# Kernel optimization log

Hardware: AMD Instinct MI355X
Metric: run time of the kernel (lower is better)

## Reference

```python
import jax, jax.numpy as jnp
import numpy as np

N = 20000
E = 320000
F_IN = 256
NHID = 64
H1 = 8
H2 = 1
NUM_CLASSES = 40
NEG_SLOPE = 0.2


def setup_inputs() -> dict:
    key = jax.random.key(0)
    ks = jax.random.split(key, 11)
    glorot = lambda k, shape: jax.random.normal(k, shape, jnp.float32) * jnp.sqrt(2.0 / (shape[0] + shape[-1]))
    x = jax.random.normal(ks[0], (N, F_IN), jnp.float32)
    edge_index = jax.random.randint(ks[1], (2, E), 0, N, jnp.int64)
    W1 = glorot(ks[2], (F_IN, H1 * NHID))
    att_src1 = glorot(ks[3], (H1, NHID))
    att_dst1 = glorot(ks[4], (H1, NHID))
    b1 = jnp.zeros((H1 * NHID,), jnp.float32)
    W2 = glorot(ks[5], (H1 * NHID, H2 * NUM_CLASSES))
    att_src2 = glorot(ks[6], (H2, NUM_CLASSES))
    att_dst2 = glorot(ks[7], (H2, NUM_CLASSES))
    b2 = jnp.zeros((NUM_CLASSES,), jnp.float32)
    return {"x": x, "edge_index": edge_index, "W1": W1, "att_src1": att_src1,
            "att_dst1": att_dst1, "b1": b1, "W2": W2, "att_src2": att_src2,
            "att_dst2": att_dst2, "b2": b2}


def gat_conv(x, src, dst, W, a_src, a_dst, bias, concat):
    # x: [N, F_in], src/dst: [E'] (self-loops already appended)
    H, C = a_src.shape
    h = (x @ W).reshape(N, H, C)                       # [N,H,C]
    alpha_src = jnp.sum(h * a_src, axis=-1)            # [N,H]
    alpha_dst = jnp.sum(h * a_dst, axis=-1)            # [N,H]
    e = jax.nn.leaky_relu(alpha_src[src] + alpha_dst[dst], NEG_SLOPE)  # [E',H]
    # segment softmax over incoming edges of each dst node
    emax = jax.lax.stop_gradient(jax.ops.segment_max(e, dst, num_segments=N))
    ee = jnp.exp(e - emax[dst])
    denom = jax.ops.segment_sum(ee, dst, num_segments=N)
    alpha = ee / (denom[dst] + 1e-16)                  # [E',H]
    out = jax.ops.segment_sum(alpha[:, :, None] * h[src], dst, num_segments=N)  # [N,H,C]
    out = out.reshape(N, H * C) if concat else out.mean(axis=1)
    return out + bias


def reference(x, edge_index, W1, att_src1, att_dst1, b1, W2, att_src2, att_dst2, b2):
    # PyG GATConv adds self-loops by default
    loops = jnp.arange(N, dtype=edge_index.dtype)
    src = jnp.concatenate([edge_index[0], loops])
    dst = jnp.concatenate([edge_index[1], loops])
    h = gat_conv(x, src, dst, W1, att_src1, att_dst1, b1, concat=True)   # [N, H1*NHID]
    h = jax.nn.elu(h)
    out = gat_conv(h, src, dst, W2, att_src2, att_dst2, b2, concat=False)  # [N, NUM_CLASSES]
    return jax.nn.log_softmax(out, axis=1)
```

## Files before the change

kernel.cpp:

```cpp
#include <hip/hip_runtime.h>
#include <hip/hip_bf16.h>
#include <math.h>

#define N_NODES 20000
#define MPAD 20096
#define N_EDGES 320000
#define EP (N_EDGES + N_NODES)
#define F_IN 256
#define NHID 64
#define H1 8
#define D1 512
#define NCLS 40
#define NEG_SLOPE 0.2f
#define MAXD 128

typedef __attribute__((ext_vector_type(8))) short bf16x8;
typedef __attribute__((ext_vector_type(4))) float f32x4;

__device__ __forceinline__ float wave_max(float v) {
#pragma unroll
  for (int o = 32; o > 0; o >>= 1) v = fmaxf(v, __shfl_xor(v, o));
  return v;
}
__device__ __forceinline__ float wave_sum(float v) {
#pragma unroll
  for (int o = 32; o > 0; o >>= 1) v += __shfl_xor(v, o);
  return v;
}
__device__ __forceinline__ unsigned short f2bf(float f) {
  union { float f; unsigned int i; } c; c.f = f;
  unsigned int x = c.i;
  return (unsigned short)((x + 0x7fffu + ((x >> 16) & 1u)) >> 16);
}
__device__ __forceinline__ float asf(unsigned int u) {
  union { unsigned int i; float f; } c; c.i = u; return c.f;
}
__device__ __forceinline__ float lrelu(float x) { return x > 0.f ? x : NEG_SLOPE * x; }

__device__ __forceinline__ void gload16(const void* g, void* l) {
  __builtin_amdgcn_global_load_lds((const __attribute__((address_space(1))) void*)g,
                                   (__attribute__((address_space(3))) void*)l, 16, 0, 0);
}

#define PB_CONV 2512
#define PB_TW1  (PB_CONV + 32)
#define PB_TW2  (PB_TW1 + 96)
#define PB_ZERO (PB_TW2 + 157)
#define PB_PAD  (PB_ZERO + 24)
__global__ __launch_bounds__(256) void prep_kernel(const float* __restrict__ x,
                                                   const float* __restrict__ W1,
                                                   const float* __restrict__ W2,
                                                   unsigned short* __restrict__ xb,
                                                   unsigned short* __restrict__ wb1t,
                                                   unsigned short* __restrict__ wb2t,
                                                   int* __restrict__ deg,
                                                   int* __restrict__ cursor,
                                                   unsigned short* __restrict__ out1b) {
  __shared__ float tsh[64][65];
  int bid = blockIdx.x;
  int t = threadIdx.x;
  if (bid < PB_CONV) {
    size_t base = ((size_t)bid * 256 + t) * 8;
    int row = (int)(base >> 8);
    ushort4 o0, o1;
    if (row < N_NODES) {
      float4 v0 = *(const float4*)&x[base];
      float4 v1 = *(const float4*)&x[base + 4];
      o0 = make_ushort4(f2bf(v0.x), f2bf(v0.y), f2bf(v0.z), f2bf(v0.w));
      o1 = make_ushort4(f2bf(v1.x), f2bf(v1.y), f2bf(v1.z), f2bf(v1.w));
    } else {
      o0 = make_ushort4(0, 0, 0, 0); o1 = o0;
    }
    *(ushort4*)&xb[base] = o0;
    *(ushort4*)&xb[base + 4] = o1;
  } else if (bid < PB_TW1) {
    int b2 = bid - PB_CONV;
    int bk = b2 & 3, bn = b2 >> 2;
    int tr = t >> 4, tc4 = (t & 15) * 4;
#pragma unroll
    for (int i = 0; i < 4; ++i) {
      int k = i * 16 + tr;
      float4 v = *(const float4*)&W1[(size_t)(bk * 64 + k) * D1 + bn * 64 + tc4];
      tsh[k][tc4] = v.x; tsh[k][tc4 + 1] = v.y; tsh[k][tc4 + 2] = v.z; tsh[k][tc4 + 3] = v.w;
    }
    __syncthreads();
#pragma unroll
    for (int i = 0; i < 4; ++i) {
      int n = i * 16 + tr;
      ushort4 o = make_ushort4(f2bf(tsh[tc4][n]), f2bf(tsh[tc4 + 1][n]),
                               f2bf(tsh[tc4 + 2][n]), f2bf(tsh[tc4 + 3][n]));
      *(ushort4*)&wb1t[(size_t)(bn * 64 + n) * F_IN + bk * 64 + tc4] = o;
    }
  } else if (bid < PB_TW2) {
    int idx = (bid - PB_TW1) * 256 + t;
    int c = idx >> 9, k = idx & 511;
    wb2t[idx] = f2bf((c < NCLS) ? W2[(size_t)k * NCLS + c] : 0.f);
  } else if (bid < PB_ZERO) {
    int idx = (bid - PB_TW2) * 256 + t;
    if (idx < N_NODES) deg[idx] = 0;
    else if (idx < 2 * N_NODES) cursor[idx - N_NODES] = 0;
  } else {
    int idx = (bid - PB_ZERO) * 256 + t;
    uint4 z = make_uint4(0, 0, 0, 0);
    *(uint4*)((char*)out1b + (size_t)N_NODES * D1 * 2 + (size_t)idx * 16) = z;
  }
}

__global__ void count_deg(const int* __restrict__ ei, int* __restrict__ deg) {
  int e = blockIdx.x * blockDim.x + threadIdx.x;
  if (e >= EP) return;
  int dst = (e < N_EDGES) ? ei[N_EDGES + e] : (e - N_EDGES);
  atomicAdd(&deg[dst], 1);
}

#define SCAN_T 1024
#define SCAN_CHUNK 20
__global__ __launch_bounds__(1024) void scan_kernel(const int* __restrict__ deg,
                                                    int* __restrict__ offsets) {
  __shared__ int wsum[16];
  int t = threadIdx.x;
  int w = t >> 6, lane = t & 63;
  int lo = t * SCAN_CHUNK;
  int hi = min(lo + SCAN_CHUNK, N_NODES);
  int s = 0;
  for (int i = lo; i < hi; ++i) s += deg[i];
  int incl = s;
#pragma unroll
  for (int o = 1; o < 64; o <<= 1) {
    int v = __shfl_up(incl, o);
    if (lane >= o) incl += v;
  }
  if (lane == 63) wsum[w] = incl;
  __syncthreads();
  if (t == 0) {
    int run = 0;
#pragma unroll
    for (int i = 0; i < 16; ++i) { int v = wsum[i]; wsum[i] = run; run += v; }
  }
  __syncthreads();
  int off = wsum[w] + incl - s;
  for (int i = lo; i < hi; ++i) { offsets[i] = off; off += deg[i]; }
  if (hi == N_NODES && lo < N_NODES) offsets[N_NODES] = off;
}

__global__ void scatter_edges(const int* __restrict__ ei, const int* __restrict__ offsets,
                              int* __restrict__ cursor, int* __restrict__ edge_src) {
  int e = blockIdx.x * blockDim.x + threadIdx.x;
  if (e >= EP) return;
  int src, dst;
  if (e < N_EDGES) { src = ei[e]; dst = ei[N_EDGES + e]; }
  else             { src = dst = e - N_EDGES; }
  int pos = offsets[dst] + atomicAdd(&cursor[dst], 1);
  edge_src[pos] = src;
}

__global__ __launch_bounds__(256) void gemm1_mfma(const unsigned short* __restrict__ xb,
                                                  const unsigned short* __restrict__ wb1t,
                                                  const float* __restrict__ a_src,
                                                  const float* __restrict__ a_dst,
                                                  unsigned short* __restrict__ h1b,
                                                  float* __restrict__ asrc,
                                                  float* __restrict__ adst) {
  __shared__ unsigned short As[128 * 64];
  __shared__ unsigned short Bs[128 * 64];
  int tid = threadIdx.x;
  int w = tid >> 6, lane = tid & 63;
  int bn = blockIdx.x & 3, bm = blockIdx.x >> 2;
  int row0 = bm * 128, col0 = bn * 128;
  int wr = w >> 1, wc = w & 1;
  int cl = lane & 15, hi = lane >> 4;
  f32x4 acc[4][4] = {};
  for (int k0 = 0; k0 < F_IN; k0 += 64) {
#pragma unroll
    for (int c = 0; c < 4; ++c) {
      int slot = c * 256 + tid;
      int r = slot >> 3;
      int q = (slot & 7) ^ (r & 7);
      gload16(xb + (size_t)(row0 + r) * F_IN + k0 + q * 8, (char*)As + (c * 256 + w * 64) * 16);
      gload16(wb1t + (size_t)(col0 + r) * F_IN + k0 + q * 8, (char*)Bs + (c * 256 + w * 64) * 16);
    }
    __syncthreads();
#pragma unroll
    for (int kk = 0; kk < 2; ++kk) {
      bf16x8 a[4], b[4];
#pragma unroll
      for (int m = 0; m < 4; ++m) {
        int r = wr * 64 + m * 16 + cl;
        a[m] = *(const bf16x8*)&As[r * 64 + ((((kk * 4 + hi)) ^ (r & 7)) << 3)];
      }
#pragma unroll
      for (int n = 0; n < 4; ++n) {
        int r = wc * 64 + n * 16 + cl;
        b[n] = *(const bf16x8*)&Bs[r * 64 + ((((kk * 4 + hi)) ^ (r & 7)) << 3)];
      }
#pragma unroll
      for (int m = 0; m < 4; ++m)
#pragma unroll
        for (int n = 0; n < 4; ++n)
          acc[m][n] = __builtin_amdgcn_mfma_f32_16x16x32_bf16(a[m], b[n], acc[m][n], 0, 0, 0);
    }
    __syncthreads();
  }
  int head = bn * 2 + wc;
  float asv[4], adv[4];
#pragma unroll
  for (int n = 0; n < 4; ++n) {
    asv[n] = a_src[head * 64 + n * 16 + cl];
    adv[n] = a_dst[head * 64 + n * 16 + cl];
  }
#pragma unroll
  for (int m = 0; m < 4; ++m) {
#pragma unroll
    for (int r = 0; r < 4; ++r) {
      int grow = row0 + wr * 64 + m * 16 + hi * 4 + r;
      float ps = acc[m][0][r] * asv[0] + acc[m][1][r] * asv[1] +
                 acc[m][2][r] * asv[2] + acc[m][3][r] * asv[3];
      float pd = acc[m][0][r] * adv[0] + acc[m][1][r] * adv[1] +
                 acc[m][2][r] * adv[2] + acc[m][3][r] * adv[3];
#pragma unroll
      for (int o = 8; o > 0; o >>= 1) { ps += __shfl_xor(ps, o); pd += __shfl_xor(pd, o); }
      if (grow < N_NODES) {
#pragma unroll
        for (int n = 0; n < 4; ++n)
          h1b[(size_t)grow * D1 + col0 + wc * 64 + n * 16 + cl] = f2bf(acc[m][n][r]);
        if (cl == 0) { asrc[grow * H1 + head] = ps; adst[grow * H1 + head] = pd; }
      }
    }
  }
}

__global__ __launch_bounds__(256) void alpha1_kernel(const int* __restrict__ offsets,
                                                     const int* __restrict__ edge_src,
                                                     const float* __restrict__ asrc,
                                                     const float* __restrict__ adst,
                                                     float* __restrict__ alphaE,
                                                     float* __restrict__ inv1) {
  int w = threadIdx.x >> 6, lane = threadIdx.x & 63;
  int n = blockIdx.x * 4 + w;
  int base = offsets[n];
  int deg = offsets[n + 1] - base;
  int h = lane & 7, et = lane >> 3;
  float adv = adst[n * H1 + h];
  float evr[8];
  float m = -INFINITY;
#pragma unroll
  for (int k = 0; k < 8; ++k) {
    int e = et + k * 8;
    float ev = -INFINITY;
    if (e < deg) ev = lrelu(asrc[edge_src[base + e] * H1 + h] + adv);
    evr[k] = ev;
    m = fmaxf(m, ev);
  }
  for (int e = et + 64; e < deg; e += 8)
    m = fmaxf(m, lrelu(asrc[edge_src[base + e] * H1 + h] + adv));
  m = fmaxf(m, __shfl_xor(m, 8));
  m = fmaxf(m, __shfl_xor(m, 16));
  m = fmaxf(m, __shfl_xor(m, 32));
  float ss = 0.f;
#pragma unroll
  for (int k = 0; k < 8; ++k) {
    int e = et + k * 8;
    if (e < deg) {
      float a = __expf(evr[k] - m);
      alphaE[(size_t)h * EP + base + e] = a;
      ss += a;
    }
  }
  for (int e = et + 64; e < deg; e += 8) {
    float a = __expf(lrelu(asrc[edge_src[base + e] * H1 + h] + adv) - m);
    alphaE[(size_t)h * EP + base + e] = a;
    ss += a;
  }
  ss += __shfl_xor(ss, 8);
  ss += __shfl_xor(ss, 16);
  ss += __shfl_xor(ss, 32);
  if (et == 0) inv1[n * H1 + h] = 1.f / (ss + 1e-16f);
}

__global__ __launch_bounds__(256) void agg1_gather(const int* __restrict__ offsets,
                                                   const int* __restrict__ edge_src,
                                                   const float* __restrict__ alphaE,
                                                   const float* __restrict__ inv1,
                                                   const unsigned short* __restrict__ h1b,
                                                   const float* __restrict__ b1,
                                                   unsigned short* __restrict__ out1b) {
  int w = threadIdx.x >> 6, lane = threadIdx.x & 63;
  int bid = blockIdx.x;
  int head = bid & 7;
  int ng = bid >> 3;
  int sub = lane >> 3, cl = lane & 7;
  int n = ng * 32 + w * 8 + sub;
  int base = offsets[n];
  int deg = offsets[n + 1] - base;
  const float* aE = alphaE + (size_t)head * EP + base;
  const int* es = edge_src + base;
  const char* hb = (const char*)h1b + head * 128 + cl * 16;
  float acc[8] = {};
  int e = 0;
  for (; e + 3 < deg; e += 4) {
    float a0 = aE[e], a1 = aE[e + 1], a2 = aE[e + 2], a3 = aE[e + 3];
    int s0 = es[e], s1 = es[e + 1], s2 = es[e + 2], s3 = es[e + 3];
    uint4 u0 = *(const uint4*)(hb + ((size_t)s0 << 10));
    uint4 u1 = *(const uint4*)(hb + ((size_t)s1 << 10));
    uint4 u2 = *(const uint4*)(hb + ((size_t)s2 << 10));
    uint4 u3 = *(const uint4*)(hb + ((size_t)s3 << 10));
#pragma unroll
    for (int j = 0; j < 4; ++j) {
      unsigned int x0 = ((const unsigned int*)&u0)[j];
      unsigned int x1 = ((const unsigned int*)&u1)[j];
      unsigned int x2 = ((const unsigned int*)&u2)[j];
      unsigned int x3 = ((const unsigned int*)&u3)[j];
      acc[2 * j]     += a0 * asf(x0 << 16) + a1 * asf(x1 << 16)
                      + a2 * asf(x2 << 16) + a3 * asf(x3 << 16);
      acc[2 * j + 1] += a0 * asf(x0 & 0xffff0000u) + a1 * asf(x1 & 0xffff0000u)
                      + a2 * asf(x2 & 0xffff0000u) + a3 * asf(x3 & 0xffff0000u);
    }
  }
  for (; e < deg; ++e) {
    float a = aE[e];
    int s = es[e];
    uint4 uv = *(const uint4*)(hb + ((size_t)s << 10));
#pragma unroll
    for (int j = 0; j < 4; ++j) {
      unsigned int u = ((const unsigned int*)&uv)[j];
      acc[2 * j]     += a * asf(u << 16);
      acc[2 * j + 1] += a * asf(u & 0xffff0000u);
    }
  }
  float inv = inv1[n * H1 + head];
  int c0 = head * NHID + cl * 8;
  float4 b0 = *(const float4*)&b1[c0];
  float4 b4 = *(const float4*)&b1[c0 + 4];
  float v[8];
  v[0] = acc[0] * inv + b0.x; v[1] = acc[1] * inv + b0.y;
  v[2] = acc[2] * inv + b0.z; v[3] = acc[3] * inv + b0.w;
  v[4] = acc[4] * inv + b4.x; v[5] = acc[5] * inv + b4.y;
  v[6] = acc[6] * inv + b4.z; v[7] = acc[7] * inv + b4.w;
#pragma unroll
  for (int j = 0; j < 8; ++j) v[j] = v[j] > 0.f ? v[j] : (__expf(v[j]) - 1.f);
  ushort4 o0 = make_ushort4(f2bf(v[0]), f2bf(v[1]), f2bf(v[2]), f2bf(v[3]));
  ushort4 o1 = make_ushort4(f2bf(v[4]), f2bf(v[5]), f2bf(v[6]), f2bf(v[7]));
  *(ushort4*)&out1b[(size_t)n * D1 + c0] = o0;
  *(ushort4*)&out1b[(size_t)n * D1 + c0 + 4] = o1;
}

__global__ __launch_bounds__(256) void gemm2_mfma(const unsigned short* __restrict__ ab,
                                                  const unsigned short* __restrict__ wb2t,
                                                  const float* __restrict__ a_src2,
                                                  const float* __restrict__ a_dst2,
                                                  float* __restrict__ h2,
                                                  float* __restrict__ asrc,
                                                  float* __restrict__ adst) {
  __shared__ unsigned short As[64 * 64];
  __shared__ unsigned short Bs[48 * 64];
  int tid = threadIdx.x;
  int w = tid >> 6, lane = tid & 63;
  int row0 = blockIdx.x * 64;
  int cl = lane & 15, hi = lane >> 4;
  f32x4 acc[3] = {};
  for (int k0 = 0; k0 < D1; k0 += 64) {
#pragma unroll
    for (int c = 0; c < 2; ++c) {
      int slot = c * 256 + tid;
      int r = slot >> 3;
      int q = (slot & 7) ^ (r & 7);
      gload16(ab + (size_t)(row0 + r) * D1 + k0 + q * 8, (char*)As + (c * 256 + w * 64) * 16);
    }
    {
      int r = tid >> 3;
      int q = (tid & 7) ^ (r & 7);
      gload16(wb2t + (size_t)r * D1 + k0 + q * 8, (char*)Bs + (w * 64) * 16);
      if (tid < 128) {
        int slot2 = 256 + tid;
        int r2 = slot2 >> 3;
        int q2 = (slot2 & 7) ^ (r2 & 7);
        gload16(wb2t + (size_t)r2 * D1 + k0 + q2 * 8, (char*)Bs + ((256 + w * 64)) * 16);
      }
    }
    __syncthreads();
#pragma unroll
    for (int kk = 0; kk < 2; ++kk) {
      int ra = w * 16 + cl;
      bf16x8 a = *(const bf16x8*)&As[ra * 64 + (((kk * 4 + hi) ^ (ra & 7)) << 3)];
#pragma unroll
      for (int n = 0; n < 3; ++n) {
        int rb = n * 16 + cl;
        bf16x8 b = *(const bf16x8*)&Bs[rb * 64 + (((kk * 4 + hi) ^ (rb & 7)) << 3)];
        acc[n] = __builtin_amdgcn_mfma_f32_16x16x32_bf16(a, b, acc[n], 0, 0, 0);
      }
    }
    __syncthreads();
  }
  float asv[3], adv[3];
#pragma unroll
  for (int n = 0; n < 3; ++n) {
    int c = n * 16 + cl;
    asv[n] = (c < NCLS) ? a_src2[c] : 0.f;
    adv[n] = (c < NCLS) ? a_dst2[c] : 0.f;
  }
#pragma unroll
  for (int r = 0; r < 4; ++r) {
    int grow = row0 + w * 16 + hi * 4 + r;
    float ps = acc[0][r] * asv[0] + acc[1][r] * asv[1] + acc[2][r] * asv[2];
    float pd = acc[0][r] * adv[0] + acc[1][r] * adv[1] + acc[2][r] * adv[2];
#pragma unroll
    for (int o = 8; o > 0; o >>= 1) { ps += __shfl_xor(ps, o); pd += __shfl_xor(pd, o); }
    if (grow < N_NODES) {
#pragma unroll
      for (int n = 0; n < 3; ++n) {
        int c = n * 16 + cl;
        if (c < NCLS) h2[(size_t)grow * NCLS + c] = acc[n][r];
      }
      if (cl == 0) { asrc[grow] = ps; adst[grow] = pd; }
    }
  }
}

__global__ __launch_bounds__(256) void agg2_kernel(const int* __restrict__ offsets,
                                                   const int* __restrict__ edge_src,
                                                   const float* __restrict__ asrc,
                                                   const float* __restrict__ adst,
                                                   const float* __restrict__ h2,
                                                   const float* __restrict__ b2,
                                                   float* __restrict__ out) {
  __shared__ float lalpha[4][MAXD + 8];
  __shared__ int   lsoff[4][MAXD + 8];
  int w = threadIdx.x >> 6;
  int lane = threadIdx.x & 63;
  int n = blockIdx.x * 4 + w;
  int base = offsets[n];
  int deg = offsets[n + 1] - base;
  int degc = min(deg, MAXD);
  int degp = ((degc + 5) / 6) * 6;

  float advv = adst[n];
  float m = -INFINITY;
  for (int e = lane; e < deg; e += 64) {
    int s = edge_src[base + e];
    float ev = lrelu(asrc[s] + advv);
    if (e < MAXD) { lsoff[w][e] = s * (NCLS * 4); lalpha[w][e] = ev; }
    m = fmaxf(m, ev);
  }
  m = wave_max(m);
  float ssum = 0.f;
  for (int e = lane; e < deg; e += 64) {
    float ev;
    if (e < MAXD) ev = lalpha[w][e];
    else { int s = edge_src[base + e]; ev = lrelu(asrc[s] + advv); }
    ssum += __expf(ev - m);
  }
  float inv = 1.f / (wave_sum(ssum) + 1e-16f);
  for (int e = lane; e < degc; e += 64) lalpha[w][e] = __expf(lalpha[w][e] - m) * inv;
  {
    int e = degc + lane;
    if (e < degp) { lalpha[w][e] = 0.f; lsoff[w][e] = 0; }
  }
  __builtin_amdgcn_wave_barrier();

  int esub = lane / 20;
  int cg = lane - esub * 20;
  bool act = esub < 3;
  float ax = 0.f, ay = 0.f;
  const char* hb = (const char*)h2 + cg * 8;
  for (int i = 0; i < degp; i += 6) {
    if (act) {
      int sA = i + esub, sB = i + 3 + esub;
      float aA = lalpha[w][sA], aB = lalpha[w][sB];
      int oA = lsoff[w][sA], oB = lsoff[w][sB];
      float2 hA = *(const float2*)(hb + oA);
      float2 hB = *(const float2*)(hb + oB);
      ax += aA * hA.x + aB * hB.x;
      ay += aA * hA.y + aB * hB.y;
    }
  }
  for (int e = MAXD + esub; e < deg; e += 3) {
    if (act) {
      int s = edge_src[base + e];
      float a = __expf(lrelu(asrc[s] + advv) - m) * inv;
      float2 hv = *(const float2*)(hb + (size_t)s * (NCLS * 4));
      ax += a * hv.x; ay += a * hv.y;
    }
  }
  float ax1 = __shfl(ax, lane + 20), ax2 = __shfl(ax, lane + 40);
  float ay1 = __shfl(ay, lane + 20), ay2 = __shfl(ay, lane + 40);
  float v0 = -INFINITY, v1 = -INFINITY;
  if (lane < 20) {
    v0 = ax + ax1 + ax2 + b2[2 * cg];
    v1 = ay + ay1 + ay2 + b2[2 * cg + 1];
  }
  float m2 = wave_max(fmaxf(v0, v1));
  float se = wave_sum(lane < 20 ? __expf(v0 - m2) + __expf(v1 - m2) : 0.f);
  if (lane < 20) {
    float ls = logf(se);
    *(float2*)&out[(size_t)n * NCLS + 2 * cg] = make_float2(v0 - m2 - ls, v1 - m2 - ls);
  }
}

extern "C" void kernel_launch(void* const* d_in, const int* in_sizes, int n_in,
                              void* d_out, int out_size, void* d_ws, size_t ws_size,
                              hipStream_t stream) {
  const float* x   = (const float*)d_in[0];
  const int*   ei  = (const int*)d_in[1];
  const float* W1  = (const float*)d_in[2];
  const float* as1 = (const float*)d_in[3];
  const float* ad1 = (const float*)d_in[4];
  const float* b1  = (const float*)d_in[5];
  const float* W2  = (const float*)d_in[6];
  const float* as2 = (const float*)d_in[7];
  const float* ad2 = (const float*)d_in[8];
  const float* b2  = (const float*)d_in[9];
  float* out = (float*)d_out;

  char* ws = (char*)d_ws;
  size_t off = 0;
  auto alloc = [&](size_t bytes) -> char* {
    char* p = ws + off;
    off += (bytes + 255) & ~(size_t)255;
    return p;
  };
  int* deg      = (int*)alloc((size_t)N_NODES * 4);
  int* cursor   = (int*)alloc((size_t)N_NODES * 4);
  int* offsets  = (int*)alloc((size_t)(N_NODES + 1) * 4);
  int* edge_src = (int*)alloc((size_t)EP * 4);
  unsigned short* xb    = (unsigned short*)alloc((size_t)MPAD * F_IN * 2);
  unsigned short* wb1t  = (unsigned short*)alloc((size_t)D1 * F_IN * 2);
  unsigned short* wb2t  = (unsigned short*)alloc((size_t)48 * D1 * 2);
  unsigned short* h1b   = (unsigned short*)alloc((size_t)N_NODES * D1 * 2);
  unsigned short* out1b = (unsigned short*)alloc((size_t)MPAD * D1 * 2);
  float* asrc1  = (float*)alloc((size_t)N_NODES * H1 * 4);
  float* adst1  = (float*)alloc((size_t)N_NODES * H1 * 4);
  float* alphaE = (float*)alloc((size_t)H1 * EP * 4);
  float* inv1   = (float*)alloc((size_t)N_NODES * H1 * 4);
  float* h2     = (float*)alloc((size_t)N_NODES * NCLS * 4);
  float* asrc2  = (float*)alloc((size_t)N_NODES * 4);
  float* adst2  = (float*)alloc((size_t)N_NODES * 4);

  prep_kernel<<<PB_PAD, 256, 0, stream>>>(x, W1, W2, xb, wb1t, wb2t, deg, cursor, out1b);
  count_deg<<<(EP + 255) / 256, 256, 0, stream>>>(ei, deg);
  scan_kernel<<<1, SCAN_T, 0, stream>>>(deg, offsets);
  scatter_edges<<<(EP + 255) / 256, 256, 0, stream>>>(ei, offsets, cursor, edge_src);

  gemm1_mfma<<<157 * 4, 256, 0, stream>>>(xb, wb1t, as1, ad1, h1b, asrc1, adst1);
  alpha1_kernel<<<N_NODES / 4, 256, 0, stream>>>(offsets, edge_src, asrc1, adst1, alphaE, inv1);
  agg1_gather<<<(N_NODES / 32) * 8, 256, 0, stream>>>(offsets, edge_src, alphaE, inv1, h1b, b1, out1b);

  gemm2_mfma<<<MPAD / 64, 256, 0, stream>>>(out1b, wb2t, as2, ad2, h2, asrc2, adst2);
  agg2_kernel<<<N_NODES / 4, 256, 0, stream>>>(offsets, edge_src, asrc2, adst2, h2, b2, out);
}
```

Before: 154.1 us.

## Sort nodes by degree for agg1 gather to balance wave work

Builds a degree histogram in the scan kernel and a new scatter_perm kernel that produces a node permutation bucketed by in-degree (capped at 63). agg1_gather processes nodes through this permutation, so the eight nodes sharing a wave have similar degrees and less lane divergence. The gather tail is also unrolled by two. This adds an extra small kernel launch and an indirection load, and scatter order within a bin is non-deterministic. Output locality is reduced because neighbouring lanes now write to scattered rows.

```diff
diff --git a/kernel.cpp b/kernel.cpp
--- a/kernel.cpp
+++ b/kernel.cpp
@@ -116,14 +116,23 @@
 #define SCAN_T 1024
 #define SCAN_CHUNK 20
 __global__ __launch_bounds__(1024) void scan_kernel(const int* __restrict__ deg,
-                                                    int* __restrict__ offsets) {
+                                                    int* __restrict__ offsets,
+                                                    int* __restrict__ binoff,
+                                                    int* __restrict__ bincur) {
   __shared__ int wsum[16];
+  __shared__ int hist[64];
   int t = threadIdx.x;
   int w = t >> 6, lane = t & 63;
+  if (t < 64) hist[t] = 0;
+  __syncthreads();
   int lo = t * SCAN_CHUNK;
   int hi = min(lo + SCAN_CHUNK, N_NODES);
   int s = 0;
-  for (int i = lo; i < hi; ++i) s += deg[i];
+  for (int i = lo; i < hi; ++i) {
+    int d = deg[i];
+    s += d;
+    atomicAdd(&hist[min(d, 63)], 1);
+  }
   int incl = s;
 #pragma unroll
   for (int o = 1; o < 64; o <<= 1) {
@@ -136,7 +145,12 @@
     int run = 0;
 #pragma unroll
     for (int i = 0; i < 16; ++i) { int v = wsum[i]; wsum[i] = run; run += v; }
-  }
+    int brun = 0;
+#pragma unroll
+    for (int i = 0; i < 64; ++i) { int v = hist[i]; binoff[i] = brun; brun += v; }
+    binoff[64] = brun;
+  }
+  if (t < 64) bincur[t] = 0;
   __syncthreads();
   int off = wsum[w] + incl - s;
   for (int i = lo; i < hi; ++i) { offsets[i] = off; off += deg[i]; }
@@ -152,6 +166,15 @@
   else             { src = dst = e - N_EDGES; }
   int pos = offsets[dst] + atomicAdd(&cursor[dst], 1);
   edge_src[pos] = src;
+}
+
+__global__ void scatter_perm(const int* __restrict__ offsets, const int* __restrict__ binoff,
+                             int* __restrict__ bincur, int* __restrict__ perm) {
+  int n = blockIdx.x * blockDim.x + threadIdx.x;
+  if (n >= N_NODES) return;
+  int d = min(offsets[n + 1] - offsets[n], 63);
+  int pos = binoff[d] + atomicAdd(&bincur[d], 1);
+  perm[pos] = n;
 }
 
 __global__ __launch_bounds__(256) void gemm1_mfma(const unsigned short* __restrict__ xb,
@@ -279,6 +302,7 @@
 
 __global__ __launch_bounds__(256) void agg1_gather(const int* __restrict__ offsets,
                                                    const int* __restrict__ edge_src,
+                                                   const int* __restrict__ perm,
                                                    const float* __restrict__ alphaE,
                                                    const float* __restrict__ inv1,
                                                    const unsigned short* __restrict__ h1b,
@@ -289,7 +313,7 @@
   int head = bid & 7;
   int ng = bid >> 3;
   int sub = lane >> 3, cl = lane & 7;
-  int n = ng * 32 + w * 8 + sub;
+  int n = perm[ng * 32 + w * 8 + sub];
   int base = offsets[n];
   int deg = offsets[n + 1] - base;
   const float* aE = alphaE + (size_t)head * EP + base;
@@ -316,7 +340,21 @@
                       + a2 * asf(x2 & 0xffff0000u) + a3 * asf(x3 & 0xffff0000u);
     }
   }
-  for (; e < deg; ++e) {
+  if (e + 1 < deg) {
+    float a0 = aE[e], a1 = aE[e + 1];
+    int s0 = es[e], s1 = es[e + 1];
+    uint4 u0 = *(const uint4*)(hb + ((size_t)s0 << 10));
+    uint4 u1 = *(const uint4*)(hb + ((size_t)s1 << 10));
+#pragma unroll
+    for (int j = 0; j < 4; ++j) {
+      unsigned int x0 = ((const unsigned int*)&u0)[j];
+      unsigned int x1 = ((const unsigned int*)&u1)[j];
+      acc[2 * j]     += a0 * asf(x0 << 16) + a1 * asf(x1 << 16);
+      acc[2 * j + 1] += a0 * asf(x0 & 0xffff0000u) + a1 * asf(x1 & 0xffff0000u);
+    }
+    e += 2;
+  }
+  if (e < deg) {
     float a = aE[e];
     int s = es[e];
     uint4 uv = *(const uint4*)(hb + ((size_t)s << 10));
@@ -522,6 +560,9 @@
   int* cursor   = (int*)alloc((size_t)N_NODES * 4);
   int* offsets  = (int*)alloc((size_t)(N_NODES + 1) * 4);
   int* edge_src = (int*)alloc((size_t)EP * 4);
+  int* binoff   = (int*)alloc(65 * 4);
+  int* bincur   = (int*)alloc(64 * 4);
+  int* perm     = (int*)alloc((size_t)N_NODES * 4);
   unsigned short* xb    = (unsigned short*)alloc((size_t)MPAD * F_IN * 2);
   unsigned short* wb1t  = (unsigned short*)alloc((size_t)D1 * F_IN * 2);
   unsigned short* wb2t  = (unsigned short*)alloc((size_t)48 * D1 * 2);
@@ -537,12 +578,13 @@
 
   prep_kernel<<<PB_PAD, 256, 0, stream>>>(x, W1, W2, xb, wb1t, wb2t, deg, cursor, out1b);
   count_deg<<<(EP + 255) / 256, 256, 0, stream>>>(ei, deg);
-  scan_kernel<<<1, SCAN_T, 0, stream>>>(deg, offsets);
+  scan_kernel<<<1, SCAN_T, 0, stream>>>(deg, offsets, binoff, bincur);
   scatter_edges<<<(EP + 255) / 256, 256, 0, stream>>>(ei, offsets, cursor, edge_src);
+  scatter_perm<<<(N_NODES + 255) / 256, 256, 0, stream>>>(offsets, binoff, bincur, perm);
 
   gemm1_mfma<<<157 * 4, 256, 0, stream>>>(xb, wb1t, as1, ad1, h1b, asrc1, adst1);
   alpha1_kernel<<<N_NODES / 4, 256, 0, stream>>>(offsets, edge_src, asrc1, adst1, alphaE, inv1);
-  agg1_gather<<<(N_NODES / 32) * 8, 256, 0, stream>>>(offsets, edge_src, alphaE, inv1, h1b, b1, out1b);
+  agg1_gather<<<(N_NODES / 32) * 8, 256, 0, stream>>>(offsets, edge_src, perm, alphaE, inv1, h1b, b1, out1b);
 
   gemm2_mfma<<<MPAD / 64, 256, 0, stream>>>(out1b, wb2t, as2, ad2, h2, asrc2, adst2);
   agg2_kernel<<<N_NODES / 4, 256, 0, stream>>>(offsets, edge_src, asrc2, adst2, h2, b2, out);
```

Result: slower. 217.2 us (+40.9%).

## Fuse degree count into prep kernel and edge scatter into gemm1 launch

Applied to the files above, without the earlier changes.

The degree-count pass moves into extra blocks of the prep kernel, and the CSR scatter moves into extra blocks of the gemm1 launch. The zeroing of deg and cursor becomes two hipMemsetAsync calls. This removes two kernel launches and lets the independent graph-building work overlap with the conversion and GEMM work. The agg1 gather loop is also unrolled to 8 edges, with 4/2/1 tails, to keep more gather loads in flight. The costs are two memset operations and heavier register use in the aggregation kernel.

```diff
diff --git a/kernel.cpp b/kernel.cpp
--- a/kernel.cpp
+++ b/kernel.cpp
@@ -45,16 +45,16 @@
 #define PB_CONV 2512
 #define PB_TW1  (PB_CONV + 32)
 #define PB_TW2  (PB_TW1 + 96)
-#define PB_ZERO (PB_TW2 + 157)
-#define PB_PAD  (PB_ZERO + 24)
+#define PB_PAD  (PB_TW2 + 24)
+#define PB_CNT  (PB_PAD + 1329)
 __global__ __launch_bounds__(256) void prep_kernel(const float* __restrict__ x,
                                                    const float* __restrict__ W1,
                                                    const float* __restrict__ W2,
+                                                   const int* __restrict__ ei,
                                                    unsigned short* __restrict__ xb,
                                                    unsigned short* __restrict__ wb1t,
                                                    unsigned short* __restrict__ wb2t,
                                                    int* __restrict__ deg,
-                                                   int* __restrict__ cursor,
                                                    unsigned short* __restrict__ out1b) {
   __shared__ float tsh[64][65];
   int bid = blockIdx.x;
@@ -95,22 +95,17 @@
     int idx = (bid - PB_TW1) * 256 + t;
     int c = idx >> 9, k = idx & 511;
     wb2t[idx] = f2bf((c < NCLS) ? W2[(size_t)k * NCLS + c] : 0.f);
-  } else if (bid < PB_ZERO) {
+  } else if (bid < PB_PAD) {
     int idx = (bid - PB_TW2) * 256 + t;
-    if (idx < N_NODES) deg[idx] = 0;
-    else if (idx < 2 * N_NODES) cursor[idx - N_NODES] = 0;
-  } else {
-    int idx = (bid - PB_ZERO) * 256 + t;
     uint4 z = make_uint4(0, 0, 0, 0);
     *(uint4*)((char*)out1b + (size_t)N_NODES * D1 * 2 + (size_t)idx * 16) = z;
-  }
-}
-
-__global__ void count_deg(const int* __restrict__ ei, int* __restrict__ deg) {
-  int e = blockIdx.x * blockDim.x + threadIdx.x;
-  if (e >= EP) return;
-  int dst = (e < N_EDGES) ? ei[N_EDGES + e] : (e - N_EDGES);
-  atomicAdd(&deg[dst], 1);
+  } else {
+    int e = (bid - PB_PAD) * 256 + t;
+    if (e < EP) {
+      int dst = (e < N_EDGES) ? ei[N_EDGES + e] : (e - N_EDGES);
+      atomicAdd(&deg[dst], 1);
+    }
+  }
 }
 
 #define SCAN_T 1024
@@ -143,27 +138,32 @@
   if (hi == N_NODES && lo < N_NODES) offsets[N_NODES] = off;
 }
 
-__global__ void scatter_edges(const int* __restrict__ ei, const int* __restrict__ offsets,
-                              int* __restrict__ cursor, int* __restrict__ edge_src) {
-  int e = blockIdx.x * blockDim.x + threadIdx.x;
-  if (e >= EP) return;
-  int src, dst;
-  if (e < N_EDGES) { src = ei[e]; dst = ei[N_EDGES + e]; }
-  else             { src = dst = e - N_EDGES; }
-  int pos = offsets[dst] + atomicAdd(&cursor[dst], 1);
-  edge_src[pos] = src;
-}
-
+#define G1_BLOCKS 628
 __global__ __launch_bounds__(256) void gemm1_mfma(const unsigned short* __restrict__ xb,
                                                   const unsigned short* __restrict__ wb1t,
                                                   const float* __restrict__ a_src,
                                                   const float* __restrict__ a_dst,
                                                   unsigned short* __restrict__ h1b,
                                                   float* __restrict__ asrc,
-                                                  float* __restrict__ adst) {
+                                                  float* __restrict__ adst,
+                                                  const int* __restrict__ ei,
+                                                  const int* __restrict__ offsets,
+                                                  int* __restrict__ cursor,
+                                                  int* __restrict__ edge_src) {
   __shared__ unsigned short As[128 * 64];
   __shared__ unsigned short Bs[128 * 64];
   int tid = threadIdx.x;
+  if (blockIdx.x >= G1_BLOCKS) {
+    int e = (blockIdx.x - G1_BLOCKS) * 256 + tid;
+    if (e < EP) {
+      int src, dst;
+      if (e < N_EDGES) { src = ei[e]; dst = ei[N_EDGES + e]; }
+      else             { src = dst = e - N_EDGES; }
+      int pos = offsets[dst] + atomicAdd(&cursor[dst], 1);
+      edge_src[pos] = src;
+    }
+    return;
+  }
   int w = tid >> 6, lane = tid & 63;
   int bn = blockIdx.x & 3, bm = blockIdx.x >> 2;
   int row0 = bm * 128, col0 = bn * 128;
@@ -297,26 +297,55 @@
   const char* hb = (const char*)h1b + head * 128 + cl * 16;
   float acc[8] = {};
   int e = 0;
+  for (; e + 7 < deg; e += 8) {
+    float av[8]; int sv[8];
+#pragma unroll
+    for (int q = 0; q < 8; ++q) { av[q] = aE[e + q]; sv[q] = es[e + q]; }
+    uint4 uv[8];
+#pragma unroll
+    for (int q = 0; q < 8; ++q) uv[q] = *(const uint4*)(hb + ((size_t)sv[q] << 10));
+#pragma unroll
+    for (int q = 0; q < 8; ++q) {
+#pragma unroll
+      for (int j = 0; j < 4; ++j) {
+        unsigned int u = ((const unsigned int*)&uv[q])[j];
+        acc[2 * j]     += av[q] * asf(u << 16);
+        acc[2 * j + 1] += av[q] * asf(u & 0xffff0000u);
+      }
+    }
+  }
   for (; e + 3 < deg; e += 4) {
-    float a0 = aE[e], a1 = aE[e + 1], a2 = aE[e + 2], a3 = aE[e + 3];
-    int s0 = es[e], s1 = es[e + 1], s2 = es[e + 2], s3 = es[e + 3];
+    float av[4]; int sv[4];
+#pragma unroll
+    for (int q = 0; q < 4; ++q) { av[q] = aE[e + q]; sv[q] = es[e + q]; }
+    uint4 uv[4];
+#pragma unroll
+    for (int q = 0; q < 4; ++q) uv[q] = *(const uint4*)(hb + ((size_t)sv[q] << 10));
+#pragma unroll
+    for (int q = 0; q < 4; ++q) {
+#pragma unroll
+      for (int j = 0; j < 4; ++j) {
+        unsigned int u = ((const unsigned int*)&uv[q])[j];
+        acc[2 * j]     += av[q] * asf(u << 16);
+        acc[2 * j + 1] += av[q] * asf(u & 0xffff0000u);
+      }
+    }
+  }
+  if (e + 1 < deg) {
+    float a0 = aE[e], a1 = aE[e + 1];
+    int s0 = es[e], s1 = es[e + 1];
     uint4 u0 = *(const uint4*)(hb + ((size_t)s0 << 10));
     uint4 u1 = *(const uint4*)(hb + ((size_t)s1 << 10));
-    uint4 u2 = *(const uint4*)(hb + ((size_t)s2 << 10));
-    uint4 u3 = *(const uint4*)(hb + ((size_t)s3 << 10));
 #pragma unroll
     for (int j = 0; j < 4; ++j) {
       unsigned int x0 = ((const unsigned int*)&u0)[j];
       unsigned int x1 = ((const unsigned int*)&u1)[j];
-      unsigned int x2 = ((const unsigned int*)&u2)[j];
-      unsigned int x3 = ((const unsigned int*)&u3)[j];
-      acc[2 * j]     += a0 * asf(x0 << 16) + a1 * asf(x1 << 16)
-                      + a2 * asf(x2 << 16) + a3 * asf(x3 << 16);
-      acc[2 * j + 1] += a0 * asf(x0 & 0xffff0000u) + a1 * asf(x1 & 0xffff0000u)
-                      + a2 * asf(x2 & 0xffff0000u) + a3 * asf(x3 & 0xffff0000u);
-    }
-  }
-  for (; e < deg; ++e) {
+      acc[2 * j]     += a0 * asf(x0 << 16) + a1 * asf(x1 << 16);
+      acc[2 * j + 1] += a0 * asf(x0 & 0xffff0000u) + a1 * asf(x1 & 0xffff0000u);
+    }
+    e += 2;
+  }
+  if (e < deg) {
     float a = aE[e];
     int s = es[e];
     uint4 uv = *(const uint4*)(hb + ((size_t)s << 10));
@@ -535,12 +564,13 @@
   float* asrc2  = (float*)alloc((size_t)N_NODES * 4);
   float* adst2  = (float*)alloc((size_t)N_NODES * 4);
 
-  prep_kernel<<<PB_PAD, 256, 0, stream>>>(x, W1, W2, xb, wb1t, wb2t, deg, cursor, out1b);
-  count_deg<<<(EP + 255) / 256, 256, 0, stream>>>(ei, deg);
+  hipMemsetAsync(deg, 0, (size_t)N_NODES * 4, stream);
+  hipMemsetAsync(cursor, 0, (size_t)N_NODES * 4, stream);
+
+  prep_kernel<<<PB_CNT, 256, 0, stream>>>(x, W1, W2, ei, xb, wb1t, wb2t, deg, out1b);
   scan_kernel<<<1, SCAN_T, 0, stream>>>(deg, offsets);
-  scatter_edges<<<(EP + 255) / 256, 256, 0, stream>>>(ei, offsets, cursor, edge_src);
-
-  gemm1_mfma<<<157 * 4, 256, 0, stream>>>(xb, wb1t, as1, ad1, h1b, asrc1, adst1);
+  gemm1_mfma<<<G1_BLOCKS + 1329, 256, 0, stream>>>(xb, wb1t, as1, ad1, h1b, asrc1, adst1,
+                                                   ei, offsets, cursor, edge_src);
   alpha1_kernel<<<N_NODES / 4, 256, 0, stream>>>(offsets, edge_src, asrc1, adst1, alphaE, inv1);
   agg1_gather<<<(N_NODES / 32) * 8, 256, 0, stream>>>(offsets, edge_src, alphaE, inv1, h1b, b1, out1b);
 
```

New measurement: 153.9 us. No clear change (-0.1%).
